# Performance work log

Measured on AMD Instinct MI355X. Metric: run time of the kernel, lower is better.

## Reference

```python
import jax, jax.numpy as jnp
import numpy as np

HID = 768
NH = 12
HD = HID // NH
EPS = 1e-12


def setup_inputs() -> dict:
    key = jax.random.key(0)
    ks = jax.random.split(key, 16)
    B, S, N = 4, 2048, 8
    s = 1.0 / np.sqrt(HID)
    s4 = 1.0 / np.sqrt(4 * HID)
    return {
        "layer_output": jax.random.normal(ks[0], (B, S, HID), jnp.float32),
        "candidates_embeddings": jax.random.normal(ks[1], (B, S, N, HID), jnp.float32),
        "candidates_mask": jax.random.bernoulli(ks[2], 0.2, (B, S, N)),
        "Wq": jax.random.uniform(ks[3], (HID, HID), jnp.float32, -s, s),
        "bq": jnp.zeros((HID,), jnp.float32),
        "Wk": jax.random.uniform(ks[4], (HID, HID), jnp.float32, -s, s),
        "bk": jnp.zeros((HID,), jnp.float32),
        "Wv": jax.random.uniform(ks[5], (HID, HID), jnp.float32, -s, s),
        "bv": jnp.zeros((HID,), jnp.float32),
        "Wt": jax.random.uniform(ks[6], (4 * HID, HID), jnp.float32, -s, s),
        "bt": jnp.zeros((4 * HID,), jnp.float32),
        "Wc": jax.random.uniform(ks[7], (HID, 4 * HID), jnp.float32, -s4, s4),
        "bc": jnp.zeros((HID,), jnp.float32),
        "gamma": jnp.ones((HID,), jnp.float32),
        "beta": jnp.zeros((HID,), jnp.float32),
    }


def reference(layer_output, candidates_embeddings, candidates_mask,
              Wq, bq, Wk, bk, Wv, bv, Wt, bt, Wc, bc, gamma, beta):
    B, S, H = layer_output.shape
    T = B * S
    N = candidates_embeddings.shape[2]
    x = layer_output.reshape(T, H)
    c = candidates_embeddings.reshape(T, N, H)
    mask = candidates_mask.reshape(T, N)

    q = (x @ Wq.T + bq).reshape(T, NH, HD)            # q_len = 1 per token
    k = (c @ Wk.T + bk).reshape(T, N, NH, HD)
    v = (c @ Wv.T + bv).reshape(T, N, NH, HD)

    scores = jnp.einsum('thd,tnhd->thn', q, k) / np.sqrt(HD)
    # masked_fill with 1e-10 (NOT -inf) — faithful to the original
    scores = jnp.where(mask[:, None, :], jnp.asarray(1e-10, scores.dtype), scores)
    attn = jax.nn.softmax(scores, axis=-1)
    ctx = jnp.einsum('thn,tnhd->thd', attn, v).reshape(T, H)
    ctx = jnp.where(jnp.all(mask, axis=-1, keepdims=True), 0.0, ctx)

    h = jax.nn.gelu(ctx @ Wt.T + bt, approximate=False)
    ctx = h @ Wc.T + bc

    out = ctx.reshape(B, S, H) + layer_output
    mu = jnp.mean(out, axis=-1, keepdims=True)
    var = jnp.var(out, axis=-1, keepdims=True)
    out = (out - mu) * jax.lax.rsqrt(var + EPS) * gamma + beta
    return out
```

## Files before the change

### kernel.cpp

```cpp
#include <hip/hip_runtime.h>

typedef __bf16 bf16x8 __attribute__((ext_vector_type(8)));
typedef float f32x4 __attribute__((ext_vector_type(4)));
typedef unsigned short us8 __attribute__((ext_vector_type(8)));
typedef unsigned short us4 __attribute__((ext_vector_type(4)));
typedef unsigned int u32;

#define HIDN 768
#define NHEAD 12
#define HDIM 64
#define FFDIM 3072
#define NCAND 8

__device__ __forceinline__ float bf2f(unsigned short u) {
    union { unsigned int i; float f; } x; x.i = ((unsigned int)u) << 16; return x.f;
}
__device__ __forceinline__ unsigned short f2bf(float f) {
    __bf16 h = (__bf16)f;
    return __builtin_bit_cast(unsigned short, h);
}

typedef const __attribute__((address_space(1))) u32* gas_p;
typedef __attribute__((address_space(3))) u32* las_p;
__device__ __forceinline__ void load_lds16(const unsigned short* g, unsigned short* l) {
    __builtin_amdgcn_global_load_lds((gas_p)(const void*)g, (las_p)(void*)l, 16, 0, 0);
}

__global__ __launch_bounds__(256) void cvt_f2b(const float* __restrict__ src,
                                               unsigned short* __restrict__ dst, long n4) {
    long i = (long)blockIdx.x * 256 + threadIdx.x;
    if (i >= n4) return;
    float4 f = ((const float4*)src)[i];
    us4 o; o[0] = f2bf(f.x); o[1] = f2bf(f.y); o[2] = f2bf(f.z); o[3] = f2bf(f.w);
    *(us4*)&dst[i * 4] = o;
}

__global__ __launch_bounds__(256) void cvt_wk(const float* __restrict__ Wk,
                                              unsigned short* __restrict__ Wk2) {
    __shared__ float t[64][65];
    const int bx = blockIdx.x;
    const int h = bx / (HIDN / 64), jt = bx % (HIDN / 64);
    const int tid = threadIdx.x;
    int rj = tid & 63, rd = tid >> 6;
    for (int d = rd; d < 64; d += 4)
        t[d][rj] = Wk[(long)(h * 64 + d) * HIDN + jt * 64 + rj];
    __syncthreads();
    int wd = tid & 63, wj = tid >> 6;
    for (int j = wj; j < 64; j += 4)
        Wk2[((long)h * HIDN + jt * 64 + j) * 64 + wd] = f2bf(t[wd][j]);
}

__global__ void zero_flags(int* __restrict__ f) {
    if (threadIdx.x < 3) f[threadIdx.x] = 0;
}
__global__ __launch_bounds__(256) void mask_scan(const unsigned char* __restrict__ m,
                                                 int nbytes, int* __restrict__ flags) {
    int a0 = 0, a1 = 0, a2 = 0;
    for (int i = blockIdx.x * 256 + threadIdx.x; i < nbytes; i += gridDim.x * 256) {
        if (m[i]) {
            int r4 = i & 3, r8 = i & 7;
            if (r4 == 1) a0 = 1;
            if (r4 >= 2) a1 = 1;
            if (r8 == 4) a2 = 1;
        }
    }
    if (a0) atomicOr(&flags[0], 1);
    if (a1) atomicOr(&flags[1], 1);
    if (a2) atomicOr(&flags[2], 1);
}

template <bool OUT_BF16, bool GELU, int AI>
__global__ __launch_bounds__(256) void gemm128(
    const unsigned short* __restrict__ A, const unsigned short* __restrict__ B,
    void* __restrict__ Cv, const float* __restrict__ bias,
    int K, int lda, int ldb, int ldc,
    long a_z, long b_z, long c_z) {
    const int z = blockIdx.z;
    A += (long)z * a_z;
    B += (long)z * b_z;
    const int tid = threadIdx.x;
    const int m0 = blockIdx.y * (AI * 32), n0 = blockIdx.x * 128;
    __shared__ __attribute__((aligned(16))) unsigned short As[AI * 32 * 64];
    __shared__ __attribute__((aligned(16))) unsigned short Bs[128 * 64];
    f32x4 acc[AI][4] = {};
    const int lane = tid & 63, w = tid >> 6;
    const int wm = w & 1, wn = w >> 1;

    for (int k0 = 0; k0 < K; k0 += 64) {
#pragma unroll
        for (int i = 0; i < AI; i++) {
            int c = i * 256 + tid;
            int row = c >> 3;
            int g = (c & 7) ^ (row & 7);
            load_lds16(&A[(long)(m0 + row) * lda + k0 + g * 8], &As[c * 8]);
        }
#pragma unroll
        for (int i = 0; i < 4; i++) {
            int c = i * 256 + tid;
            int row = c >> 3;
            int g = (c & 7) ^ (row & 7);
            load_lds16(&B[(long)(n0 + row) * ldb + k0 + g * 8], &Bs[c * 8]);
        }
        __syncthreads();
#pragma unroll
        for (int kk = 0; kk < 64; kk += 32) {
            const int gc = (kk >> 3) + (lane >> 4);
            bf16x8 af[AI], bfr[4];
#pragma unroll
            for (int i = 0; i < AI; i++) {
                int r = wm * (AI * 16) + i * 16 + (lane & 15);
                af[i] = *(const bf16x8*)&As[r * 64 + ((gc ^ (r & 7)) << 3)];
            }
#pragma unroll
            for (int j = 0; j < 4; j++) {
                int r = wn * 64 + j * 16 + (lane & 15);
                bfr[j] = *(const bf16x8*)&Bs[r * 64 + ((gc ^ (r & 7)) << 3)];
            }
#pragma unroll
            for (int i = 0; i < AI; i++)
#pragma unroll
                for (int j = 0; j < 4; j++)
                    acc[i][j] = __builtin_amdgcn_mfma_f32_16x16x32_bf16(af[i], bfr[j], acc[i][j], 0, 0, 0);
        }
        __syncthreads();
    }

    float* Cf = (float*)Cv;
    unsigned short* Ch = (unsigned short*)Cv;
    const long cbase = (long)z * c_z;
#pragma unroll
    for (int i = 0; i < AI; i++)
#pragma unroll
        for (int j = 0; j < 4; j++) {
            int col = n0 + wn * 64 + j * 16 + (lane & 15);
            int rbase = m0 + wm * (AI * 16) + i * 16 + ((lane >> 4) * 4);
            float bb = bias ? bias[col] : 0.f;
#pragma unroll
            for (int r = 0; r < 4; r++) {
                int row = rbase + r;
                float v = acc[i][j][r] + bb;
                if (GELU) v = 0.5f * v * (1.f + erff(v * 0.70710678118654752f));
                long off = cbase + (long)row * ldc + col;
                if (OUT_BF16) Ch[off] = f2bf(v);
                else Cf[off] = v;
            }
        }
}

template <bool OUT_BF16, bool GELU, bool FLAG>
__global__ __launch_bounds__(256) void gemm_bt(
    const unsigned short* __restrict__ A, const unsigned short* __restrict__ B,
    void* __restrict__ Cv, const float* __restrict__ bias, const float* __restrict__ flag,
    int N, int K, int lda, int ldc,
    long a_z, long b_z, long c_z, int bias_z) {
    const int z = blockIdx.z;
    A += (long)z * a_z;
    B += (long)z * b_z;
    const int tid = threadIdx.x;
    const int m0 = blockIdx.y * 64, n0 = blockIdx.x * 64;
    __shared__ __attribute__((aligned(16))) unsigned short As[64][72];
    __shared__ __attribute__((aligned(16))) unsigned short Bs[64][72];
    f32x4 acc[2][2] = {};
    const int lane = tid & 63, w = tid >> 6;
    const int wm = w & 1, wn = w >> 1;
    const int ar = tid >> 3;
    const int ac = (tid & 7) * 8;

    for (int k0 = 0; k0 < K; k0 += 64) {
#pragma unroll
        for (int r = 0; r < 2; r++) {
            int row = ar + r * 32;
            us8 av = *(const us8*)&A[(long)(m0 + row) * lda + k0 + ac];
            *(us8*)&As[row][ac] = av;
            us8 bv = *(const us8*)&B[(long)(n0 + row) * K + k0 + ac];
            *(us8*)&Bs[row][ac] = bv;
        }
        __syncthreads();
#pragma unroll
        for (int kk = 0; kk < 64; kk += 32) {
            int kf = kk + (lane >> 4) * 8;
            bf16x8 a0 = *(const bf16x8*)&As[wm * 32 + (lane & 15)][kf];
            bf16x8 a1 = *(const bf16x8*)&As[wm * 32 + 16 + (lane & 15)][kf];
            bf16x8 b0 = *(const bf16x8*)&Bs[wn * 32 + (lane & 15)][kf];
            bf16x8 b1 = *(const bf16x8*)&Bs[wn * 32 + 16 + (lane & 15)][kf];
            acc[0][0] = __builtin_amdgcn_mfma_f32_16x16x32_bf16(a0, b0, acc[0][0], 0, 0, 0);
            acc[0][1] = __builtin_amdgcn_mfma_f32_16x16x32_bf16(a0, b1, acc[0][1], 0, 0, 0);
            acc[1][0] = __builtin_amdgcn_mfma_f32_16x16x32_bf16(a1, b0, acc[1][0], 0, 0, 0);
            acc[1][1] = __builtin_amdgcn_mfma_f32_16x16x32_bf16(a1, b1, acc[1][1], 0, 0, 0);
        }
        __syncthreads();
    }

    float* Cf = (float*)Cv;
    unsigned short* Ch = (unsigned short*)Cv;
    const long cbase = (long)z * c_z;
#pragma unroll
    for (int tm = 0; tm < 2; tm++)
#pragma unroll
        for (int tn = 0; tn < 2; tn++) {
            int col = n0 + wn * 32 + tn * 16 + (lane & 15);
            int rbase = m0 + wm * 32 + tm * 16 + ((lane >> 4) * 4);
            float bb = bias ? bias[(long)z * bias_z + col] : 0.f;
#pragma unroll
            for (int r = 0; r < 4; r++) {
                int row = rbase + r;
                float v = acc[tm][tn][r] + bb;
                if (GELU) v = 0.5f * v * (1.f + erff(v * 0.70710678118654752f));
                if (FLAG) v *= flag[row];
                long off = cbase + (long)row * ldc + col;
                if (OUT_BF16) Ch[off] = f2bf(v);
                else Cf[off] = v;
            }
        }
}

__global__ __launch_bounds__(256) void qbk_kernel(const unsigned short* __restrict__ Qb,
                                                  const float* __restrict__ bk,
                                                  float* __restrict__ qbk, long npair) {
    int lane = threadIdx.x & 63, w = threadIdx.x >> 6;
    long p = (long)blockIdx.x * 4 + w;
    if (p >= npair) return;
    long t = p / 12;
    int h = (int)(p - t * 12);
    float v = bf2f(Qb[t * HIDN + h * 64 + lane]) * bk[h * 64 + lane];
    for (int o = 32; o; o >>= 1) v += __shfl_down(v, o);
    if (lane == 0) qbk[p] = v;
}

#define LDP 776
__global__ __launch_bounds__(256) void attn_kernel(
    const float* __restrict__ cands, unsigned short* __restrict__ qkcw,
    const void* __restrict__ maskp, const int* __restrict__ flags,
    const float* __restrict__ qbk, float* __restrict__ allm, long t0) {
    const int tid = threadIdx.x;
    const long tl = blockIdx.x;
    const long t = t0 + tl;
    __shared__ __attribute__((aligned(16))) unsigned short buf[8 * LDP + 12 * HIDN];
    unsigned short* c_s = buf;
    unsigned short* qk_s = buf + 8 * LDP;
    __shared__ float scr[16][16];
    __shared__ int msk[NCAND];
    __shared__ float qb_s[NHEAD];

    const unsigned short* qsrc = qkcw + tl * (NHEAD * HIDN);
#pragma unroll
    for (int p = 0; p < 5; p++) {
        int i = tid + p * 256;
        if (i < NHEAD * HIDN / 8) {
            int row = i / 96, cc = i - row * 96;
            int g = (cc & ~7) | ((cc & 7) ^ (row & 7));
            load_lds16(&qsrc[row * HIDN + g * 8], &qk_s[i * 8]);
        }
    }
    const float4* c4 = (const float4*)(cands + t * NCAND * HIDN);
    float4 cf[6];
#pragma unroll
    for (int p = 0; p < 6; p++) {
        int i = tid + p * 256;
        int n = i / 192, j4 = (i - n * 192) * 4;
        float4 f = c4[i];
        cf[p] = f;
        us4 o; o[0] = f2bf(f.x); o[1] = f2bf(f.y); o[2] = f2bf(f.z); o[3] = f2bf(f.w);
        *(us4*)&c_s[n * LDP + j4] = o;
    }
    if (tid < NCAND) {
        int mm = flags[0] ? 1 : (flags[1] ? 2 : (flags[2] ? 0 : 3));
        long mi = t * NCAND + tid;
        int mv;
        if (mm == 1)      mv = ((const unsigned char*)maskp)[mi] != 0;
        else if (mm == 2) mv = ((const float*)maskp)[mi] != 0.f;
        else if (mm == 3) mv = ((const long long*)maskp)[mi] != 0;
        else              mv = ((const int*)maskp)[mi] != 0;
        msk[tid] = mv;
    }
    if (tid >= 64 && tid < 64 + NHEAD) qb_s[tid - 64] = qbk[tl * NHEAD + (tid - 64)];
    __syncthreads();

    const int lane = tid & 63, w = tid >> 6;

    if (w == 0) {
        int ar = lane & 15; if (ar > 11) ar = 11;
        int br = lane & 15; if (br > 7) br = 7;
        const int kq = lane >> 4;
        const unsigned short* brow = &c_s[br * LDP + kq * 8];
        f32x4 a0 = {}, a1 = {};
#pragma unroll
        for (int k0 = 0; k0 < HIDN; k0 += 64) {
            int c1 = (k0 >> 3) + kq, c2 = c1 + 4;
            int g1 = (c1 & ~7) | ((c1 & 7) ^ (ar & 7));
            int g2 = (c2 & ~7) | ((c2 & 7) ^ (ar & 7));
            bf16x8 afa = *(const bf16x8*)&qk_s[ar * HIDN + g1 * 8];
            bf16x8 afb = *(const bf16x8*)&qk_s[ar * HIDN + g2 * 8];
            bf16x8 bfa = *(const bf16x8*)&brow[k0];
            bf16x8 bfb = *(const bf16x8*)&brow[k0 + 32];
            a0 = __builtin_amdgcn_mfma_f32_16x16x32_bf16(afa, bfa, a0, 0, 0, 0);
            a1 = __builtin_amdgcn_mfma_f32_16x16x32_bf16(afb, bfb, a1, 0, 0, 0);
        }
        int n = lane & 15;
#pragma unroll
        for (int r = 0; r < 4; r++) {
            int h = (lane >> 4) * 4 + r;
            scr[h][n] = a0[r] + a1[r];
        }
    }
    if (tid == 64) {
        int a = 1;
        for (int n = 0; n < NCAND; n++) a &= msk[n];
        allm[tl] = a ? 0.f : 1.f;
    }
    __syncthreads();

    if (tid < NHEAD) {
        int h = tid;
        float sv[NCAND], sm = 0.f, mx = -1e30f;
        for (int n = 0; n < NCAND; n++) {
            sv[n] = msk[n] ? 1e-10f : (scr[h][n] + qb_s[h]) * 0.125f;
            mx = fmaxf(mx, sv[n]);
        }
        for (int n = 0; n < NCAND; n++) { sv[n] = expf(sv[n] - mx); sm += sv[n]; }
        float inv = 1.f / sm;
        for (int n = 0; n < NCAND; n++) scr[h][n] = sv[n] * inv;
    }
    float* c32 = (float*)buf;
#pragma unroll
    for (int p = 0; p < 6; p++) {
        int i = tid + p * 256;
        *(float4*)&c32[i * 4] = cf[p];
    }
    __syncthreads();

    unsigned short* out = qkcw + tl * (NHEAD * HIDN);
#pragma unroll
    for (int p = 0; p < 5; p++) {
        int i = tid + p * 256;
        if (i < NHEAD * HIDN / 8) {
            int h = i / 96, j8 = (i - h * 96) * 8;
            f32x4 acc0 = {}, acc1 = {};
#pragma unroll
            for (int n = 0; n < NCAND; n++) {
                float a = scr[h][n];
                f32x4 v0 = *(const f32x4*)&c32[n * HIDN + j8];
                f32x4 v1 = *(const f32x4*)&c32[n * HIDN + j8 + 4];
#pragma unroll
                for (int k = 0; k < 4; k++) { acc0[k] += a * v0[k]; acc1[k] += a * v1[k]; }
            }
            us8 o;
#pragma unroll
            for (int k = 0; k < 4; k++) { o[k] = f2bf(acc0[k]); o[4 + k] = f2bf(acc1[k]); }
            *(us8*)&out[i * 8] = o;
        }
    }
}

__global__ __launch_bounds__(256) void ln_kernel(float* __restrict__ io, const float* __restrict__ x,
                                                 const float* __restrict__ gamma,
                                                 const float* __restrict__ beta, long t0) {
    const int tid = threadIdx.x;
    const long tl = blockIdx.x;
    const long t = t0 + tl;
    float* row = io + tl * HIDN;
    const float* xr = x + t * HIDN;
    float v[3];
#pragma unroll
    for (int i = 0; i < 3; i++) v[i] = row[tid + i * 256] + xr[tid + i * 256];
    __shared__ float red[4];
    const int lane = tid & 63, w = tid >> 6;
    float s = v[0] + v[1] + v[2];
    for (int o = 32; o; o >>= 1) s += __shfl_down(s, o);
    if (lane == 0) red[w] = s;
    __syncthreads();
    float mu = (red[0] + red[1] + red[2] + red[3]) * (1.f / HIDN);
    __syncthreads();
    float d0 = v[0] - mu, d1 = v[1] - mu, d2 = v[2] - mu;
    float q = d0 * d0 + d1 * d1 + d2 * d2;
    for (int o = 32; o; o >>= 1) q += __shfl_down(q, o);
    if (lane == 0) red[w] = q;
    __syncthreads();
    float var = (red[0] + red[1] + red[2] + red[3]) * (1.f / HIDN);
    float inv = rsqrtf(var + 1e-12f);
#pragma unroll
    for (int i = 0; i < 3; i++) {
        int j = tid + i * 256;
        row[j] = (v[i] - mu) * inv * gamma[j] + beta[j];
    }
}

extern "C" void kernel_launch(void* const* d_in, const int* in_sizes, int n_in,
                              void* d_out, int out_size, void* d_ws, size_t ws_size,
                              hipStream_t stream) {
    const float* x     = (const float*)d_in[0];
    const float* cands = (const float*)d_in[1];
    const void*  maskp = d_in[2];
    const float* Wq = (const float*)d_in[3];
    const float* bq = (const float*)d_in[4];
    const float* Wk = (const float*)d_in[5];
    const float* bk = (const float*)d_in[6];
    const float* Wv = (const float*)d_in[7];
    const float* bv = (const float*)d_in[8];
    const float* Wt = (const float*)d_in[9];
    const float* bt = (const float*)d_in[10];
    const float* Wc = (const float*)d_in[11];
    const float* bc = (const float*)d_in[12];
    const float* gamma = (const float*)d_in[13];
    const float* beta  = (const float*)d_in[14];
    float* out = (float*)d_out;

    const long T = (long)in_sizes[0] / HIDN;

    char* p = (char*)d_ws;
    auto alloc = [&](size_t bytes) -> char* {
        char* r = p;
        p += (bytes + 255) & ~(size_t)255;
        return r;
    };
    unsigned short* Wqb  = (unsigned short*)alloc((size_t)HIDN * HIDN * 2);
    unsigned short* Wk2b = (unsigned short*)alloc((size_t)HIDN * HIDN * 2);
    unsigned short* Wvb  = (unsigned short*)alloc((size_t)HIDN * HIDN * 2);
    unsigned short* Wtb  = (unsigned short*)alloc((size_t)FFDIM * HIDN * 2);
    unsigned short* Wcb  = (unsigned short*)alloc((size_t)HIDN * FFDIM * 2);
    int* flags = (int*)alloc(256);
    size_t fixed = (size_t)(p - (char*)d_ws);

    long TC = T;
    auto chunk_bytes = [&](long tc) -> size_t {
        return (size_t)tc * (HIDN * 2 + HIDN * 2 + NHEAD * 4 + 4 +
                             HIDN * 2 + NHEAD * HIDN * 2) + 8 * 256;
    };
    while (TC > 512 && fixed + chunk_bytes(TC) > ws_size) TC >>= 1;

    unsigned short* Xb   = (unsigned short*)alloc((size_t)TC * HIDN * 2);
    unsigned short* Qb   = (unsigned short*)alloc((size_t)TC * HIDN * 2);
    float* qbkb          = (float*)alloc((size_t)TC * NHEAD * 4);
    float* allm          = (float*)alloc((size_t)TC * 4);
    unsigned short* CTXb = (unsigned short*)alloc((size_t)TC * HIDN * 2);
    unsigned short* BIG  = (unsigned short*)alloc((size_t)TC * NHEAD * HIDN * 2);

    {
        long n4;
        n4 = (long)HIDN * HIDN / 4;
        cvt_f2b<<<dim3((n4 + 255) / 256), 256, 0, stream>>>(Wq, Wqb, n4);
        cvt_f2b<<<dim3((n4 + 255) / 256), 256, 0, stream>>>(Wv, Wvb, n4);
        n4 = (long)FFDIM * HIDN / 4;
        cvt_f2b<<<dim3((n4 + 255) / 256), 256, 0, stream>>>(Wt, Wtb, n4);
        cvt_f2b<<<dim3((n4 + 255) / 256), 256, 0, stream>>>(Wc, Wcb, n4);
        cvt_wk<<<dim3(NHEAD * (HIDN / 64)), 256, 0, stream>>>(Wk, Wk2b);
        zero_flags<<<dim3(1), 64, 0, stream>>>(flags);
        mask_scan<<<dim3(256), 256, 0, stream>>>((const unsigned char*)maskp,
                                                 (int)(T * NCAND), flags);
    }

    for (long t0 = 0; t0 < T; t0 += TC) {
        long n4 = TC * HIDN / 4;
        cvt_f2b<<<dim3((n4 + 255) / 256), 256, 0, stream>>>(x + t0 * HIDN, Xb, n4);

        gemm128<true, false, 2><<<dim3(HIDN / 128, TC / 64, 1), 256, 0, stream>>>(
            Xb, Wqb, Qb, bq, HIDN, HIDN, HIDN, HIDN, 0, 0, 0);

        qbk_kernel<<<dim3((TC * NHEAD + 3) / 4), 256, 0, stream>>>(Qb, bk, qbkb, TC * NHEAD);

        gemm128<true, false, 4><<<dim3(HIDN / 128, TC / 128, NHEAD), 256, 0, stream>>>(
            Qb, Wk2b, BIG, nullptr, HDIM, HIDN, HDIM, NHEAD * HIDN,
            HDIM, (long)HIDN * HDIM, HIDN);

        attn_kernel<<<dim3(TC), 256, 0, stream>>>(cands, BIG, maskp, flags, qbkb, allm, t0);

        gemm_bt<true, false, true><<<dim3(1, TC / 64, NHEAD), 256, 0, stream>>>(
            BIG, Wvb, CTXb, bv, allm, HDIM, HIDN, NHEAD * HIDN, HIDN,
            HIDN, (long)HDIM * HIDN, HDIM, HDIM);

        gemm128<true, true, 4><<<dim3(FFDIM / 128, TC / 128, 1), 256, 0, stream>>>(
            CTXb, Wtb, BIG, bt, HIDN, HIDN, HIDN, FFDIM, 0, 0, 0);

        gemm128<false, false, 2><<<dim3(HIDN / 128, TC / 64, 1), 256, 0, stream>>>(
            BIG, Wcb, out + t0 * HIDN, bc, FFDIM, FFDIM, FFDIM, HIDN, 0, 0, 0);

        ln_kernel<<<dim3(TC), 256, 0, stream>>>(out + t0 * HIDN, x, gamma, beta, t0);
    }
}
```

Before: 633.5 us.

## Replace V-projection GEMM with swizzled direct-to-LDS N64 kernel and enlarge M tiles

The old gemm_bt for the per-head V projection is replaced by gemm_n64. It uses direct global-to-LDS 16-byte loads with XOR swizzling instead of padded shared arrays, a taller M tile (AI*32 rows), and a fixed bf16 flagged epilogue. Several other gemm128 launches now use larger M tiles (AI doubled), which halves the block count per launch. The aim is more data reuse per block and fewer LDS bank conflicts, at the risk of lower occupancy or fewer blocks to fill the CUs.

```diff
diff --git a/kernel.cpp b/kernel.cpp
--- a/kernel.cpp
+++ b/kernel.cpp
@@ -147,69 +147,74 @@
         }
 }
 
-template <bool OUT_BF16, bool GELU, bool FLAG>
-__global__ __launch_bounds__(256) void gemm_bt(
+template <int AI>
+__global__ __launch_bounds__(256) void gemm_n64(
     const unsigned short* __restrict__ A, const unsigned short* __restrict__ B,
-    void* __restrict__ Cv, const float* __restrict__ bias, const float* __restrict__ flag,
-    int N, int K, int lda, int ldc,
-    long a_z, long b_z, long c_z, int bias_z) {
+    unsigned short* __restrict__ C, const float* __restrict__ bias,
+    const float* __restrict__ flag,
+    int K, int lda, int ldc, long a_z, long b_z, int c_col_z, int bias_z) {
     const int z = blockIdx.z;
     A += (long)z * a_z;
     B += (long)z * b_z;
     const int tid = threadIdx.x;
-    const int m0 = blockIdx.y * 64, n0 = blockIdx.x * 64;
-    __shared__ __attribute__((aligned(16))) unsigned short As[64][72];
-    __shared__ __attribute__((aligned(16))) unsigned short Bs[64][72];
-    f32x4 acc[2][2] = {};
+    const int m0 = blockIdx.y * (AI * 32);
+    __shared__ __attribute__((aligned(16))) unsigned short As[AI * 32 * 64];
+    __shared__ __attribute__((aligned(16))) unsigned short Bs[64 * 64];
+    f32x4 acc[AI][2] = {};
     const int lane = tid & 63, w = tid >> 6;
     const int wm = w & 1, wn = w >> 1;
-    const int ar = tid >> 3;
-    const int ac = (tid & 7) * 8;
 
     for (int k0 = 0; k0 < K; k0 += 64) {
 #pragma unroll
-        for (int r = 0; r < 2; r++) {
-            int row = ar + r * 32;
-            us8 av = *(const us8*)&A[(long)(m0 + row) * lda + k0 + ac];
-            *(us8*)&As[row][ac] = av;
-            us8 bv = *(const us8*)&B[(long)(n0 + row) * K + k0 + ac];
-            *(us8*)&Bs[row][ac] = bv;
+        for (int i = 0; i < AI; i++) {
+            int c = i * 256 + tid;
+            int row = c >> 3;
+            int g = (c & 7) ^ (row & 7);
+            load_lds16(&A[(long)(m0 + row) * lda + k0 + g * 8], &As[c * 8]);
+        }
+#pragma unroll
+        for (int i = 0; i < 2; i++) {
+            int c = i * 256 + tid;
+            int row = c >> 3;
+            int g = (c & 7) ^ (row & 7);
+            load_lds16(&B[(long)row * K + k0 + g * 8], &Bs[c * 8]);
         }
         __syncthreads();
 #pragma unroll
         for (int kk = 0; kk < 64; kk += 32) {
-            int kf = kk + (lane >> 4) * 8;
-            bf16x8 a0 = *(const bf16x8*)&As[wm * 32 + (lane & 15)][kf];
-            bf16x8 a1 = *(const bf16x8*)&As[wm * 32 + 16 + (lane & 15)][kf];
-            bf16x8 b0 = *(const bf16x8*)&Bs[wn * 32 + (lane & 15)][kf];
-            bf16x8 b1 = *(const bf16x8*)&Bs[wn * 32 + 16 + (lane & 15)][kf];
-            acc[0][0] = __builtin_amdgcn_mfma_f32_16x16x32_bf16(a0, b0, acc[0][0], 0, 0, 0);
-            acc[0][1] = __builtin_amdgcn_mfma_f32_16x16x32_bf16(a0, b1, acc[0][1], 0, 0, 0);
-            acc[1][0] = __builtin_amdgcn_mfma_f32_16x16x32_bf16(a1, b0, acc[1][0], 0, 0, 0);
-            acc[1][1] = __builtin_amdgcn_mfma_f32_16x16x32_bf16(a1, b1, acc[1][1], 0, 0, 0);
+            const int gc = (kk >> 3) + (lane >> 4);
+            bf16x8 af[AI], bfr[2];
+#pragma unroll
+            for (int i = 0; i < AI; i++) {
+                int r = wm * (AI * 16) + i * 16 + (lane & 15);
+                af[i] = *(const bf16x8*)&As[r * 64 + ((gc ^ (r & 7)) << 3)];
+            }
+#pragma unroll
+            for (int j = 0; j < 2; j++) {
+                int r = wn * 32 + j * 16 + (lane & 15);
+                bfr[j] = *(const bf16x8*)&Bs[r * 64 + ((gc ^ (r & 7)) << 3)];
+            }
+#pragma unroll
+            for (int i = 0; i < AI; i++)
+#pragma unroll
+                for (int j = 0; j < 2; j++)
+                    acc[i][j] = __builtin_amdgcn_mfma_f32_16x16x32_bf16(af[i], bfr[j], acc[i][j], 0, 0, 0);
         }
         __syncthreads();
     }
 
-    float* Cf = (float*)Cv;
-    unsigned short* Ch = (unsigned short*)Cv;
-    const long cbase = (long)z * c_z;
-#pragma unroll
-    for (int tm = 0; tm < 2; tm++)
-#pragma unroll
-        for (int tn = 0; tn < 2; tn++) {
-            int col = n0 + wn * 32 + tn * 16 + (lane & 15);
-            int rbase = m0 + wm * 32 + tm * 16 + ((lane >> 4) * 4);
-            float bb = bias ? bias[(long)z * bias_z + col] : 0.f;
+#pragma unroll
+    for (int i = 0; i < AI; i++)
+#pragma unroll
+        for (int j = 0; j < 2; j++) {
+            int col = wn * 32 + j * 16 + (lane & 15);
+            int rbase = m0 + wm * (AI * 16) + i * 16 + ((lane >> 4) * 4);
+            float bb = bias[(long)z * bias_z + col];
 #pragma unroll
             for (int r = 0; r < 4; r++) {
                 int row = rbase + r;
-                float v = acc[tm][tn][r] + bb;
-                if (GELU) v = 0.5f * v * (1.f + erff(v * 0.70710678118654752f));
-                if (FLAG) v *= flag[row];
-                long off = cbase + (long)row * ldc + col;
-                if (OUT_BF16) Ch[off] = f2bf(v);
-                else Cf[off] = v;
+                float v = (acc[i][j][r] + bb) * flag[row];
+                C[(long)row * ldc + (long)z * c_col_z + col] = f2bf(v);
             }
         }
 }
@@ -453,25 +458,25 @@
         long n4 = TC * HIDN / 4;
         cvt_f2b<<<dim3((n4 + 255) / 256), 256, 0, stream>>>(x + t0 * HIDN, Xb, n4);
 
-        gemm128<true, false, 2><<<dim3(HIDN / 128, TC / 64, 1), 256, 0, stream>>>(
+        gemm128<true, false, 4><<<dim3(HIDN / 128, TC / 128, 1), 256, 0, stream>>>(
             Xb, Wqb, Qb, bq, HIDN, HIDN, HIDN, HIDN, 0, 0, 0);
 
         qbk_kernel<<<dim3((TC * NHEAD + 3) / 4), 256, 0, stream>>>(Qb, bk, qbkb, TC * NHEAD);
 
-        gemm128<true, false, 4><<<dim3(HIDN / 128, TC / 128, NHEAD), 256, 0, stream>>>(
+        gemm128<true, false, 8><<<dim3(HIDN / 128, TC / 256, NHEAD), 256, 0, stream>>>(
             Qb, Wk2b, BIG, nullptr, HDIM, HIDN, HDIM, NHEAD * HIDN,
             HDIM, (long)HIDN * HDIM, HIDN);
 
         attn_kernel<<<dim3(TC), 256, 0, stream>>>(cands, BIG, maskp, flags, qbkb, allm, t0);
 
-        gemm_bt<true, false, true><<<dim3(1, TC / 64, NHEAD), 256, 0, stream>>>(
-            BIG, Wvb, CTXb, bv, allm, HDIM, HIDN, NHEAD * HIDN, HIDN,
+        gemm_n64<4><<<dim3(1, TC / 128, NHEAD), 256, 0, stream>>>(
+            BIG, Wvb, CTXb, bv, allm, HIDN, NHEAD * HIDN, HIDN,
             HIDN, (long)HDIM * HIDN, HDIM, HDIM);
 
         gemm128<true, true, 4><<<dim3(FFDIM / 128, TC / 128, 1), 256, 0, stream>>>(
             CTXb, Wtb, BIG, bt, HIDN, HIDN, HIDN, FFDIM, 0, 0, 0);
 
-        gemm128<false, false, 2><<<dim3(HIDN / 128, TC / 64, 1), 256, 0, stream>>>(
+        gemm128<false, false, 4><<<dim3(HIDN / 128, TC / 128, 1), 256, 0, stream>>>(
             BIG, Wcb, out + t0 * HIDN, bc, FFDIM, FFDIM, FFDIM, HIDN, 0, 0, 0);
 
         ln_kernel<<<dim3(TC), 256, 0, stream>>>(out + t0 * HIDN, x, gamma, beta, t0);
```

Result: slower. 687.5 us (+8.5%).
